# Kernel tuning notes

Measured on AMD Instinct MI355X. Metric: run time of the kernel, lower is better.

Reference implementation:

```python
import jax, jax.numpy as jnp
import numpy as np
import math

B, T, D, H = 2, 2048, 1024, 16
DH = D // H


def setup_inputs() -> dict:
    key = jax.random.key(0)
    k1, k2, k3 = jax.random.split(key, 3)
    scale_in = 1.0 / math.sqrt(D)
    x = jax.random.normal(k1, (B, T, D), dtype=jnp.float32)
    w_qkv = jax.random.normal(k2, (D, 3 * D), dtype=jnp.float32) * scale_in
    b_qkv = jnp.zeros((3 * D,), dtype=jnp.float32)
    w_out = jax.random.normal(k3, (D, D), dtype=jnp.float32) * scale_in
    b_out = jnp.zeros((D,), dtype=jnp.float32)
    return {"x": x, "w_qkv": w_qkv, "b_qkv": b_qkv, "w_out": w_out, "b_out": b_out}


def reference(x, w_qkv, b_qkv, w_out, b_out):
    # Fused QKV projection: [B,T,3D]
    qkv = x @ w_qkv + b_qkv
    q, k, v = jnp.split(qkv, 3, axis=-1)
    # [B,H,T,DH]
    q = q.reshape(B, T, H, DH).transpose(0, 2, 1, 3)
    k = k.reshape(B, T, H, DH).transpose(0, 2, 1, 3)
    v = v.reshape(B, T, H, DH).transpose(0, 2, 1, 3)
    # scores: [B,H,T,T]
    scores = jnp.einsum('bhqd,bhkd->bhqk', q, k) / math.sqrt(DH)
    causal_mask = jnp.tril(jnp.ones((T, T), dtype=bool))
    scores = jnp.where(causal_mask, scores, -1e10)
    attn = jax.nn.softmax(scores, axis=-1)
    out = jnp.einsum('bhqk,bhkd->bhqd', attn, v)
    out = out.transpose(0, 2, 1, 3).reshape(B, T, D)
    return out @ w_out + b_out
```

## Files before the change

### kernel.cpp

```cpp
#include <hip/hip_runtime.h>
#include <hip/hip_bf16.h>
#include <stdint.h>

#define Bsz  2
#define Tseq 2048
#define Dmod 1024
#define Hn   16
#define DHd  64

typedef short bf16x8 __attribute__((ext_vector_type(8)));
typedef float f32x4 __attribute__((ext_vector_type(4)));

__device__ __forceinline__ float bf2f(unsigned short u) {
  union { unsigned int i; float f; } v; v.i = ((unsigned int)u) << 16; return v.f;
}
__device__ __forceinline__ unsigned short f2bf(float f) {
  union { float f; unsigned int i; } v; v.f = f;
  unsigned int r = (v.i + 0x7fffu + ((v.i >> 16) & 1u)) >> 16;
  return (unsigned short)r;
}
__device__ __forceinline__ unsigned int pk_bf16(float a, float b) {
  union { __hip_bfloat162 h; unsigned int u; } u2;
  u2.h = __float22bfloat162_rn(make_float2(a, b));
  return u2.u;
}
__device__ __forceinline__ void gl_lds16(const unsigned short* g, unsigned short* l) {
  __builtin_amdgcn_global_load_lds(
      (const __attribute__((address_space(1))) void*)g,
      (__attribute__((address_space(3))) void*)l, 16, 0, 0);
}

#define QSCALE 0.1803368801f

__global__ __launch_bounds__(256) void prep(const float* __restrict__ x,
                                            const float* __restrict__ w_qkv,
                                            const float* __restrict__ w_out,
                                            unsigned short* __restrict__ xb,
                                            unsigned short* __restrict__ wqkvT,
                                            unsigned short* __restrict__ woutT) {
  __shared__ unsigned short tile[64][65];
  const int blk = blockIdx.x;
  if (blk < 2048) {
    int idx = blk * 2048 + threadIdx.x * 8;
    float4 a = *(const float4*)&x[idx];
    float4 b = *(const float4*)&x[idx + 4];
    unsigned short o[8];
    o[0] = f2bf(a.x); o[1] = f2bf(a.y); o[2] = f2bf(a.z); o[3] = f2bf(a.w);
    o[4] = f2bf(b.x); o[5] = f2bf(b.y); o[6] = f2bf(b.z); o[7] = f2bf(b.w);
    *(uint4*)&xb[idx] = *(const uint4*)o;
    return;
  }
  const float* in;
  unsigned short* out;
  int K = 1024, N, k0, n0;
  if (blk < 2048 + 768) {
    int t = blk - 2048;
    in = w_qkv; out = wqkvT; N = 3072;
    n0 = (t % 48) * 64; k0 = (t / 48) * 64;
  } else {
    int t = blk - 2816;
    in = w_out; out = woutT; N = 1024;
    n0 = (t % 16) * 64; k0 = (t / 16) * 64;
  }
  for (int i = threadIdx.x * 4; i < 4096; i += 1024) {
    int r = i >> 6, c = i & 63;
    float4 f = *(const float4*)&in[(size_t)(k0 + r) * N + n0 + c];
    tile[r][c]     = f2bf(f.x);
    tile[r][c + 1] = f2bf(f.y);
    tile[r][c + 2] = f2bf(f.z);
    tile[r][c + 3] = f2bf(f.w);
  }
  __syncthreads();
  for (int i = threadIdx.x * 8; i < 4096; i += 2048) {
    int r = i >> 6, c = i & 63;
    unsigned short o[8];
#pragma unroll
    for (int j = 0; j < 8; j++) o[j] = tile[c + j][r];
    *(uint4*)&out[(size_t)(n0 + r) * K + k0 + c] = *(const uint4*)o;
  }
}

template<int MT, int NT>
__global__ __launch_bounds__(256) void gemm_bt(const unsigned short* __restrict__ A,
                                               const unsigned short* __restrict__ Bt,
                                               const float* __restrict__ bias,
                                               int M, int N, int K, int mode,
                                               float* __restrict__ outF,
                                               unsigned short* __restrict__ out0,
                                               unsigned short* __restrict__ out1,
                                               unsigned short* __restrict__ out2) {
  constexpr int IT = MT / 32;
  constexpr int JT = NT / 32;
  constexpr int AP = MT / 64;
  constexpr int BP = NT / 64;
  __shared__ unsigned short As[2][MT * 32];
  __shared__ unsigned short Bs[2][NT * 32];
  const int tid  = threadIdx.x;
  const int lane = tid & 63;
  const int w    = tid >> 6;
  const int m0   = blockIdx.x * MT;
  const int n0   = blockIdx.y * NT;
  const int wr   = (w >> 1) * (MT / 2);
  const int wc   = (w & 1) * (NT / 2);

  f32x4 acc[IT][JT];
  for (int i = 0; i < IT; i++)
    for (int j = 0; j < JT; j++)
      for (int v = 0; v < 4; v++) acc[i][j][v] = 0.0f;

  const int l16  = lane & 15;
  const int g    = lane >> 4;
  const int fkey = (l16 & 3) ^ ((l16 >> 2) & 3);

  const int csw = (((lane & 3) ^ ((lane >> 2) & 3) ^ ((lane >> 4) & 3)) & 3) * 8;
  const unsigned short* ga[AP];
  const unsigned short* gb[BP];
  unsigned short* la[2][AP];
  unsigned short* lb[2][BP];
#pragma unroll
  for (int p = 0; p < AP; p++) {
    int r = (MT / 4) * w + 16 * p + (lane >> 2);
    ga[p] = A + (size_t)(m0 + r) * K + csw;
    la[0][p] = &As[0][((MT / 4) * w + 16 * p) * 32];
    la[1][p] = &As[1][((MT / 4) * w + 16 * p) * 32];
  }
#pragma unroll
  for (int p = 0; p < BP; p++) {
    int r = (NT / 4) * w + 16 * p + (lane >> 2);
    gb[p] = Bt + (size_t)(n0 + r) * K + csw;
    lb[0][p] = &Bs[0][((NT / 4) * w + 16 * p) * 32];
    lb[1][p] = &Bs[1][((NT / 4) * w + 16 * p) * 32];
  }

#pragma unroll
  for (int p = 0; p < AP; p++) gl_lds16(ga[p], la[0][p]);
#pragma unroll
  for (int p = 0; p < BP; p++) gl_lds16(gb[p], lb[0][p]);
  __syncthreads();

  for (int kt = 0; kt < K; kt += 32) {
    const int cur = (kt >> 5) & 1, nxt = cur ^ 1;
    if (kt + 32 < K) {
#pragma unroll
      for (int p = 0; p < AP; p++) gl_lds16(ga[p] + kt + 32, la[nxt][p]);
#pragma unroll
      for (int p = 0; p < BP; p++) gl_lds16(gb[p] + kt + 32, lb[nxt][p]);
    }
    bf16x8 af[IT], bf[JT];
#pragma unroll
    for (int i = 0; i < IT; i++)
      af[i] = *(const bf16x8*)&As[cur][(wr + i * 16 + l16) * 32 + ((g ^ fkey) * 8)];
#pragma unroll
    for (int j = 0; j < JT; j++)
      bf[j] = *(const bf16x8*)&Bs[cur][(wc + j * 16 + l16) * 32 + ((g ^ fkey) * 8)];
#pragma unroll
    for (int i = 0; i < IT; i++)
#pragma unroll
      for (int j = 0; j < JT; j++)
        acc[i][j] = __builtin_amdgcn_mfma_f32_16x16x32_bf16(af[i], bf[j], acc[i][j], 0, 0, 0);
    __syncthreads();
  }

  const int q4 = g * 4;
#pragma unroll
  for (int i = 0; i < IT; i++)
#pragma unroll
    for (int j = 0; j < JT; j++) {
      const int mbase = m0 + wr + i * 16 + q4;
      const int n = n0 + wc + j * 16 + l16;
      float vals[4];
#pragma unroll
      for (int v = 0; v < 4; v++) vals[v] = acc[i][j][v] + bias[n];
      if (mode == 1) {
#pragma unroll
        for (int v = 0; v < 4; v++)
          outF[(size_t)(mbase + v) * N + n] = vals[v];
      } else {
        const int which = n >> 10;
        const int rem = n & 1023;
        const int h = rem >> 6, dd = rem & 63;
        const int b = mbase >> 11, t = mbase & 2047;
        if (which == 2) {
          uint2 uu;
          uu.x = pk_bf16(vals[0], vals[1]);
          uu.y = pk_bf16(vals[2], vals[3]);
          const int t2 = (t & ~63) | (t & 32) | (((t >> 2) & 3) << 3) | (((t >> 4) & 1) << 2);
          *(uint2*)&out2[((size_t)((b * Hn + h) * DHd + dd)) * Tseq + t2] = uu;
        } else if (which == 0) {
#pragma unroll
          for (int v = 0; v < 4; v++)
            out0[(size_t)((b * Hn + h) * Tseq + t + v) * DHd + dd] = f2bf(vals[v] * QSCALE);
        } else {
#pragma unroll
          for (int v = 0; v < 4; v++)
            out1[(size_t)((b * Hn + h) * Tseq + t + v) * DHd + dd] = f2bf(vals[v]);
        }
      }
    }
}

__global__ __launch_bounds__(256) void gemm_bt2(const unsigned short* __restrict__ A,
                                                const unsigned short* __restrict__ Bt,
                                                const float* __restrict__ bias,
                                                int M, int N, int K,
                                                float* __restrict__ outF) {
  __shared__ unsigned short As[2][64 * 64];
  __shared__ unsigned short Bs[2][64 * 64];
  const int tid  = threadIdx.x;
  const int lane = tid & 63;
  const int w    = tid >> 6;
  const int m0   = blockIdx.x * 64;
  const int n0   = blockIdx.y * 64;
  const int wr   = (w >> 1) * 32;
  const int wc   = (w & 1) * 32;
  const int l16  = lane & 15;
  const int g    = lane >> 4;
  const int swz  = l16 & 7;

  f32x4 acc[2][2];
  for (int i = 0; i < 2; i++)
    for (int j = 0; j < 2; j++)
      for (int v = 0; v < 4; v++) acc[i][j][v] = 0.f;

  const int csw = (((lane & 7) ^ (lane >> 3)) & 7) * 8;
  const unsigned short* ga[2];
  const unsigned short* gb[2];
  unsigned short* la[2][2];
  unsigned short* lb[2][2];
#pragma unroll
  for (int p = 0; p < 2; p++) {
    const int r = 16 * w + 8 * p + (lane >> 3);
    ga[p] = A  + (size_t)(m0 + r) * K + csw;
    gb[p] = Bt + (size_t)(n0 + r) * K + csw;
    la[0][p] = &As[0][(16 * w + 8 * p) * 64];
    la[1][p] = &As[1][(16 * w + 8 * p) * 64];
    lb[0][p] = &Bs[0][(16 * w + 8 * p) * 64];
    lb[1][p] = &Bs[1][(16 * w + 8 * p) * 64];
  }

#pragma unroll
  for (int p = 0; p < 2; p++) { gl_lds16(ga[p], la[0][p]); gl_lds16(gb[p], lb[0][p]); }
  __syncthreads();

  for (int kt = 0; kt < K; kt += 64) {
    const int cur = (kt >> 6) & 1, nxt = cur ^ 1;
    if (kt + 64 < K) {
#pragma unroll
      for (int p = 0; p < 2; p++) {
        gl_lds16(ga[p] + kt + 64, la[nxt][p]);
        gl_lds16(gb[p] + kt + 64, lb[nxt][p]);
      }
    }
#pragma unroll
    for (int ks = 0; ks < 2; ks++) {
      bf16x8 af[2], bf[2];
#pragma unroll
      for (int i = 0; i < 2; i++)
        af[i] = *(const bf16x8*)&As[cur][(wr + i * 16 + l16) * 64 + (((ks * 4 + g) ^ swz) * 8)];
#pragma unroll
      for (int j = 0; j < 2; j++)
        bf[j] = *(const bf16x8*)&Bs[cur][(wc + j * 16 + l16) * 64 + (((ks * 4 + g) ^ swz) * 8)];
#pragma unroll
      for (int i = 0; i < 2; i++)
#pragma unroll
        for (int j = 0; j < 2; j++)
          acc[i][j] = __builtin_amdgcn_mfma_f32_16x16x32_bf16(af[i], bf[j], acc[i][j], 0, 0, 0);
    }
    __syncthreads();
  }

  const int q4 = g * 4;
#pragma unroll
  for (int i = 0; i < 2; i++)
#pragma unroll
    for (int j = 0; j < 2; j++) {
      const int mbase = m0 + wr + i * 16 + q4;
      const int n = n0 + wc + j * 16 + l16;
#pragma unroll
      for (int v = 0; v < 4; v++)
        outF[(size_t)(mbase + v) * N + n] = acc[i][j][v] + bias[n];
    }
}

__global__ __launch_bounds__(256, 4) void attn_mfma(const unsigned short* __restrict__ Qb,
                                                    const unsigned short* __restrict__ Kb,
                                                    const unsigned short* __restrict__ Vtg,
                                                    unsigned short* __restrict__ O) {
  __shared__ unsigned short Ks[2][64 * 64];
  __shared__ unsigned short Vs[2][64 * 64];

  const int tid  = threadIdx.x;
  const int lane = tid & 63;
  const int w    = tid >> 6;
  const int g    = lane >> 4;
  const int l16  = lane & 15;
  const int bh   = blockIdx.x;
  const int tile = (int)gridDim.y - 1 - (int)blockIdx.y;
  const int q0w  = tile * 64 + w * 16;

  const unsigned short* Qp = Qb  + (size_t)bh * Tseq * DHd;
  const unsigned short* Kp = Kb  + (size_t)bh * Tseq * DHd;
  const unsigned short* Vp = Vtg + (size_t)bh * DHd * Tseq;

  bf16x8 qf[2];
#pragma unroll
  for (int ks = 0; ks < 2; ks++)
    qf[ks] = *(const bf16x8*)&Qp[(size_t)(q0w + l16) * DHd + ks * 32 + g * 8];

  f32x4 Oacc[4];
#pragma unroll
  for (int dt = 0; dt < 4; dt++)
#pragma unroll
    for (int v = 0; v < 4; v++) Oacc[dt][v] = 0.f;

  const f32x4 FZ = {0.f, 0.f, 0.f, 0.f};
  f32x4 Lacc = {0.f, 0.f, 0.f, 0.f};
  bf16x8 onef;
  {
    union { unsigned short s[8]; bf16x8 v8; } ou;
#pragma unroll
    for (int m = 0; m < 8; m++) ou.s[m] = 0x3F80;
    onef = ou.v8;
  }
  const int swz = l16 & 7;

  const int csw = (((lane & 7) ^ (lane >> 3)) & 7) * 8;
  const unsigned short* KgB = Kp + (size_t)(16 * w + (lane >> 3)) * DHd + csw;
  const unsigned short* VgB = Vp + (size_t)(16 * w + (lane >> 3)) * Tseq + csw;
  unsigned short* KsW[2] = { &Ks[0][16 * w * 64], &Ks[1][16 * w * 64] };
  unsigned short* VsW[2] = { &Vs[0][16 * w * 64], &Vs[1][16 * w * 64] };

  gl_lds16(KgB,             KsW[0]);
  gl_lds16(KgB + 8 * DHd,   KsW[0] + 8 * 64);
  gl_lds16(VgB,             VsW[0]);
  gl_lds16(VgB + 8 * Tseq,  VsW[0] + 8 * 64);
  __syncthreads();

  for (int c = 0; c <= tile; c++) {
    const int cur = c & 1, nxt = cur ^ 1;
    if (c < tile) {
      const size_t ko = (size_t)(c + 1) * 64 * DHd;
      const int    vo = (c + 1) * 64;
      gl_lds16(KgB + ko,            KsW[nxt]);
      gl_lds16(KgB + ko + 8 * DHd,  KsW[nxt] + 8 * 64);
      gl_lds16(VgB + vo,            VsW[nxt]);
      gl_lds16(VgB + vo + 8 * Tseq, VsW[nxt] + 8 * 64);
    }

    f32x4 st[4];
    {
      bf16x8 kf[4];
#pragma unroll
      for (int mt = 0; mt < 4; mt++)
        kf[mt] = *(const bf16x8*)&Ks[cur][(16 * mt + l16) * 64 + ((g ^ swz) * 8)];
      __builtin_amdgcn_s_setprio(1);
#pragma unroll
      for (int mt = 0; mt < 4; mt++)
        st[mt] = __builtin_amdgcn_mfma_f32_16x16x32_bf16(kf[mt], qf[0], FZ, 0, 0, 0);
      __builtin_amdgcn_s_setprio(0);
    }
    {
      bf16x8 kf[4];
#pragma unroll
      for (int mt = 0; mt < 4; mt++)
        kf[mt] = *(const bf16x8*)&Ks[cur][(16 * mt + l16) * 64 + (((4 + g) ^ swz) * 8)];
      __builtin_amdgcn_s_setprio(1);
#pragma unroll
      for (int mt = 0; mt < 4; mt++)
        st[mt] = __builtin_amdgcn_mfma_f32_16x16x32_bf16(kf[mt], qf[1], st[mt], 0, 0, 0);
      __builtin_amdgcn_s_setprio(0);
    }

    if (c == tile) {
      const int qg = q0w + l16;
#pragma unroll
      for (int mt = 0; mt < 4; mt++)
#pragma unroll
        for (int v = 0; v < 4; v++)
          if ((c * 64 + 16 * mt + 4 * g + v) > qg) st[mt][v] = -1e30f;
    }

    unsigned int pw[2][4];
#pragma unroll
    for (int mt = 0; mt < 4; mt++) {
      float p[4];
#pragma unroll
      for (int v = 0; v < 4; v++) p[v] = __builtin_exp2f(st[mt][v]);
      pw[mt >> 1][(mt & 1) * 2 + 0] = pk_bf16(p[0], p[1]);
      pw[mt >> 1][(mt & 1) * 2 + 1] = pk_bf16(p[2], p[3]);
    }

#pragma unroll
    for (int ks = 0; ks < 2; ks++) {
      union { unsigned int u[4]; bf16x8 v8; } pu;
#pragma unroll
      for (int m = 0; m < 4; m++) pu.u[m] = pw[ks][m];
      const bf16x8 pf = pu.v8;
      bf16x8 vf[4];
#pragma unroll
      for (int dt = 0; dt < 4; dt++)
        vf[dt] = *(const bf16x8*)&Vs[cur][(16 * dt + l16) * 64 + (((4 * ks + g) ^ swz) * 8)];
      __builtin_amdgcn_s_setprio(1);
      Lacc = __builtin_amdgcn_mfma_f32_16x16x32_bf16(pf, onef, Lacc, 0, 0, 0);
#pragma unroll
      for (int dt = 0; dt < 4; dt++)
        Oacc[dt] = __builtin_amdgcn_mfma_f32_16x16x32_bf16(pf, vf[dt], Oacc[dt], 0, 0, 0);
      __builtin_amdgcn_s_setprio(0);
    }

    __syncthreads();
  }

  const float i0 = 1.f / Lacc[0], i1 = 1.f / Lacc[1];
  const float i2 = 1.f / Lacc[2], i3 = 1.f / Lacc[3];
  const int b = bh >> 4, h = bh & 15;
#pragma unroll
  for (int dt = 0; dt < 4; dt++) {
    const int d = h * DHd + 16 * dt + l16;
    const size_t r0 = (size_t)(b * Tseq + q0w + 4 * g) * Dmod + d;
    O[r0]            = f2bf(Oacc[dt][0] * i0);
    O[r0 + Dmod]     = f2bf(Oacc[dt][1] * i1);
    O[r0 + 2 * Dmod] = f2bf(Oacc[dt][2] * i2);
    O[r0 + 3 * Dmod] = f2bf(Oacc[dt][3] * i3);
  }
}

extern "C" void kernel_launch(void* const* d_in, const int* in_sizes, int n_in,
                              void* d_out, int out_size, void* d_ws, size_t ws_size,
                              hipStream_t stream) {
  (void)in_sizes; (void)n_in; (void)out_size; (void)ws_size;
  const float* x     = (const float*)d_in[0];
  const float* w_qkv = (const float*)d_in[1];
  const float* b_qkv = (const float*)d_in[2];
  const float* w_out = (const float*)d_in[3];
  const float* b_out = (const float*)d_in[4];
  float* out = (float*)d_out;

  unsigned short* ws    = (unsigned short*)d_ws;
  unsigned short* xb    = ws;
  unsigned short* wqkvT = xb    + (size_t)4194304;
  unsigned short* woutT = wqkvT + (size_t)3072 * 1024;
  unsigned short* Qb    = woutT + (size_t)1024 * 1024;
  unsigned short* Kb    = Qb + (size_t)4194304;
  unsigned short* Vt    = Kb + (size_t)4194304;
  unsigned short* Ob    = xb;

  prep<<<3072, 256, 0, stream>>>(x, w_qkv, w_out, xb, wqkvT, woutT);
  gemm_bt<128, 128><<<dim3(32, 24), 256, 0, stream>>>(xb, wqkvT, b_qkv, 4096, 3072, 1024, 0,
                                                      nullptr, Qb, Kb, Vt);
  attn_mfma<<<dim3(32, 32), 256, 0, stream>>>(Qb, Kb, Vt, Ob);
  gemm_bt2<<<dim3(64, 16), 256, 0, stream>>>(Ob, woutT, b_out, 4096, 1024, 1024, out);
}
```

Measured before the change: 172.6 us.

## Triple-buffer GEMM LDS staging with two-stage-ahead prefetch and partial vmcnt waits

Moves the bf16 GEMM's shared-memory staging from double to triple buffering, so global-to-LDS loads are issued two K-steps ahead. The full __syncthreads is replaced by a partial s_waitcnt vmcnt plus an explicit s_barrier, so the block only waits for the tile it needs next. This is meant to hide more global-load latency behind MFMA work. In exchange it uses 1.5x the LDS, which can lower occupancy. The hardcoded vmcnt(4) assumes four loads per stage, which holds only for some MT/NT instantiations.

```diff
diff --git a/kernel.cpp b/kernel.cpp
--- a/kernel.cpp
+++ b/kernel.cpp
@@ -93,8 +93,8 @@
   constexpr int JT = NT / 32;
   constexpr int AP = MT / 64;
   constexpr int BP = NT / 64;
-  __shared__ unsigned short As[2][MT * 32];
-  __shared__ unsigned short Bs[2][NT * 32];
+  __shared__ unsigned short As[3][MT * 32];
+  __shared__ unsigned short Bs[3][NT * 32];
   const int tid  = threadIdx.x;
   const int lane = tid & 63;
   const int w    = tid >> 6;
@@ -115,36 +115,43 @@
   const int csw = (((lane & 3) ^ ((lane >> 2) & 3) ^ ((lane >> 4) & 3)) & 3) * 8;
   const unsigned short* ga[AP];
   const unsigned short* gb[BP];
-  unsigned short* la[2][AP];
-  unsigned short* lb[2][BP];
+  unsigned short* la[3][AP];
+  unsigned short* lb[3][BP];
 #pragma unroll
   for (int p = 0; p < AP; p++) {
     int r = (MT / 4) * w + 16 * p + (lane >> 2);
     ga[p] = A + (size_t)(m0 + r) * K + csw;
-    la[0][p] = &As[0][((MT / 4) * w + 16 * p) * 32];
-    la[1][p] = &As[1][((MT / 4) * w + 16 * p) * 32];
+#pragma unroll
+    for (int b = 0; b < 3; b++) la[b][p] = &As[b][((MT / 4) * w + 16 * p) * 32];
   }
 #pragma unroll
   for (int p = 0; p < BP; p++) {
     int r = (NT / 4) * w + 16 * p + (lane >> 2);
     gb[p] = Bt + (size_t)(n0 + r) * K + csw;
-    lb[0][p] = &Bs[0][((NT / 4) * w + 16 * p) * 32];
-    lb[1][p] = &Bs[1][((NT / 4) * w + 16 * p) * 32];
+#pragma unroll
+    for (int b = 0; b < 3; b++) lb[b][p] = &Bs[b][((NT / 4) * w + 16 * p) * 32];
   }
 
 #pragma unroll
   for (int p = 0; p < AP; p++) gl_lds16(ga[p], la[0][p]);
 #pragma unroll
   for (int p = 0; p < BP; p++) gl_lds16(gb[p], lb[0][p]);
-  __syncthreads();
-
+#pragma unroll
+  for (int p = 0; p < AP; p++) gl_lds16(ga[p] + 32, la[1][p]);
+#pragma unroll
+  for (int p = 0; p < BP; p++) gl_lds16(gb[p] + 32, lb[1][p]);
+  asm volatile("s_waitcnt vmcnt(4)" ::: "memory");
+  __builtin_amdgcn_sched_barrier(0);
+  __builtin_amdgcn_s_barrier();
+
+  int cur = 0;
   for (int kt = 0; kt < K; kt += 32) {
-    const int cur = (kt >> 5) & 1, nxt = cur ^ 1;
-    if (kt + 32 < K) {
-#pragma unroll
-      for (int p = 0; p < AP; p++) gl_lds16(ga[p] + kt + 32, la[nxt][p]);
-#pragma unroll
-      for (int p = 0; p < BP; p++) gl_lds16(gb[p] + kt + 32, lb[nxt][p]);
+    const int pre = (cur == 0) ? 2 : cur - 1;
+    if (kt + 64 < K) {
+#pragma unroll
+      for (int p = 0; p < AP; p++) gl_lds16(ga[p] + kt + 64, la[pre][p]);
+#pragma unroll
+      for (int p = 0; p < BP; p++) gl_lds16(gb[p] + kt + 64, lb[pre][p]);
     }
     bf16x8 af[IT], bf[JT];
 #pragma unroll
@@ -158,7 +165,14 @@
 #pragma unroll
       for (int j = 0; j < JT; j++)
         acc[i][j] = __builtin_amdgcn_mfma_f32_16x16x32_bf16(af[i], bf[j], acc[i][j], 0, 0, 0);
-    __syncthreads();
+    if (kt + 64 < K) {
+      asm volatile("s_waitcnt vmcnt(4)" ::: "memory");
+    } else {
+      asm volatile("s_waitcnt vmcnt(0)" ::: "memory");
+    }
+    __builtin_amdgcn_sched_barrier(0);
+    __builtin_amdgcn_s_barrier();
+    cur = (cur == 2) ? 0 : cur + 1;
   }
 
   const int q4 = g * 4;
```

Result: slower. 176.6 us (+2.3%).
